# Performance work log

Hardware: AMD Instinct MI355X
Metric: run time of the kernel (lower is better)

Reference implementation:

```python
import jax, jax.numpy as jnp
import numpy as np

N_QUBITS = 4
N_LAYERS = 2
BATCH = 262144


def _apply_ry(psi, theta, wire):
    # psi: (B, 2,2,2,2) real statevector; theta: scalar or (B,)
    c = jnp.reshape(jnp.cos(theta * 0.5), (-1, 1, 1, 1))
    s = jnp.reshape(jnp.sin(theta * 0.5), (-1, 1, 1, 1))
    psi = jnp.moveaxis(psi, wire + 1, 1)
    a, b = psi[:, 0], psi[:, 1]
    psi = jnp.stack([c * a - s * b, s * a + c * b], axis=1)
    return jnp.moveaxis(psi, 1, wire + 1)


def _apply_cnot(psi, ctrl, tgt):
    # flip target amplitude where control bit is 1
    psi = jnp.moveaxis(psi, (ctrl + 1, tgt + 1), (1, 2))
    psi = psi.at[:, 1].set(psi[:, 1, ::-1])
    return jnp.moveaxis(psi, (1, 2), (ctrl + 1, tgt + 1))


def _circuit(encoded, q_params):
    # Batched 4-qubit statevector sim (RY/CNOT are real matrices -> real psi).
    B = encoded.shape[0]
    psi = jnp.zeros((B, 2 ** N_QUBITS), encoded.dtype).at[:, 0].set(1.0)
    psi = psi.reshape((B,) + (2,) * N_QUBITS)  # wire 0 = most significant axis
    for w in range(N_QUBITS):
        psi = _apply_ry(psi, encoded[:, w], w)
    for layer in range(N_LAYERS):
        for i in range(N_QUBITS - 1):
            psi = _apply_cnot(psi, i, i + 1)
        psi = _apply_cnot(psi, N_QUBITS - 1, 0)  # ring closure (n_qubits > 2)
        for i in range(N_QUBITS):
            psi = _apply_ry(psi, q_params[layer * N_QUBITS + i], i)
    p = psi * psi  # probabilities
    zs = []
    for w in range(N_QUBITS):
        pw = jnp.moveaxis(p, w + 1, 1).reshape(B, 2, -1)
        zs.append(pw[:, 0].sum(-1) - pw[:, 1].sum(-1))  # <Z_w>
    return jnp.stack(zs, axis=-1)  # (B, 4)


def setup_inputs() -> dict:
    key = jax.random.key(0)
    ks = jax.random.split(key, 10)
    f32 = jnp.float32
    state = jax.random.normal(ks[0], (BATCH, 64), dtype=f32)
    # state_encoder: Linear(64,32) -> ReLU -> Linear(32,4) -> Tanh
    W1 = jax.random.normal(ks[1], (32, 64), dtype=f32) / np.sqrt(64.0)
    b1 = jnp.zeros((32,), f32)
    W2 = jax.random.normal(ks[2], (N_QUBITS, 32), dtype=f32) / np.sqrt(32.0)
    b2 = jnp.zeros((N_QUBITS,), f32)
    q_params = jax.random.normal(ks[3], (N_LAYERS * N_QUBITS,), dtype=f32) * 0.1
    # q_value_head: Linear(4,32) -> ReLU -> Linear(32,16) -> Tanh
    H1 = jax.random.normal(ks[4], (32, N_QUBITS), dtype=f32) / np.sqrt(float(N_QUBITS))
    c1 = jnp.zeros((32,), f32)
    H2 = jax.random.normal(ks[5], (16, 32), dtype=f32) / np.sqrt(32.0)
    c2 = jnp.zeros((16,), f32)
    return {"state": state, "W1": W1, "b1": b1, "W2": W2, "b2": b2,
            "q_params": q_params, "H1": H1, "c1": c1, "H2": H2, "c2": c2}


def reference(state, W1, b1, W2, b2, q_params, H1, c1, H2, c2):
    B = state.shape[0]
    x = state.reshape(B, -1)
    h = jax.nn.relu(x @ W1.T + b1)
    encoded = jnp.tanh(h @ W2.T + b2)            # (B, 4) rotation angles
    qf = _circuit(encoded, q_params)             # (B, 4) PauliZ expectations
    h2 = jax.nn.relu(qf @ H1.T + c1)
    q_values = jnp.tanh(h2 @ H2.T + c2)          # (B, 16)
    return q_values.reshape(B, 4, 4)
```

## Files before the change

### kernel.cpp

```cpp
#include <hip/hip_runtime.h>
#include <hip/hip_bf16.h>

#define TPB 256
#define BATCH 262144

__device__ __forceinline__ float fast_tanh(float x) {
    float ax = fabsf(x);
    float e  = __expf(-2.0f * ax);
    float t  = (1.0f - e) / (1.0f + e);
    return copysignf(t, x);
}

template <int MASK>
__device__ __forceinline__ void ry_gate(float* psi, float c, float s) {
#pragma unroll
    for (int i = 0; i < 16; i++) {
        if (!(i & MASK)) {
            float a = psi[i], b = psi[i | MASK];
            psi[i]        = c * a - s * b;
            psi[i | MASK] = s * a + c * b;
        }
    }
}

template <int CM, int TM>
__device__ __forceinline__ void cnot_gate(float* psi) {
#pragma unroll
    for (int i = 0; i < 16; i++) {
        if ((i & CM) && !(i & TM)) {
            float t = psi[i];
            psi[i] = psi[i | TM];
            psi[i | TM] = t;
        }
    }
}

__global__ __launch_bounds__(TPB) void qnet_kernel(
    const float* __restrict__ state,
    const float* __restrict__ W1, const float* __restrict__ b1,
    const float* __restrict__ W2, const float* __restrict__ b2,
    const float* __restrict__ qp,
    const float* __restrict__ H1, const float* __restrict__ c1,
    const float* __restrict__ H2, const float* __restrict__ c2,
    float* __restrict__ out)
{
    __shared__ float sW1[2048];
    __shared__ float sb1[32];
    __shared__ float sW2[128];
    __shared__ float sb2[4];
    __shared__ float sH1[128];
    __shared__ float sc1[32];
    __shared__ float sH2[512];
    __shared__ float sc2[16];
    __shared__ float sQc[8], sQs[8];

    const int tid = threadIdx.x;
    for (int i = tid; i < 2048; i += TPB) sW1[i] = W1[i];
    for (int i = tid; i < 512;  i += TPB) sH2[i] = H2[i];
    if (tid < 128) { sW2[tid] = W2[tid]; sH1[tid] = H1[tid]; }
    if (tid < 32)  { sb1[tid] = b1[tid]; sc1[tid] = c1[tid]; }
    if (tid < 16)  { sc2[tid] = c2[tid]; }
    if (tid < 4)   { sb2[tid] = b2[tid]; }
    if (tid < 8) {
        float s, c;
        __sincosf(0.5f * qp[tid], &s, &c);
        sQs[tid] = s; sQc[tid] = c;
    }
    __syncthreads();

    const int bidx = blockIdx.x * TPB + tid;

    float h[32];
#pragma unroll
    for (int j = 0; j < 32; j++) h[j] = sb1[j];

    const float4* x4 = reinterpret_cast<const float4*>(state + (size_t)bidx * 64);

#pragma unroll
    for (int ic = 0; ic < 4; ic++) {
        float4 xr[4];
#pragma unroll
        for (int k = 0; k < 4; k++) xr[k] = x4[ic * 4 + k];

#pragma unroll
        for (int j = 0; j < 32; j++) {
            const float4* w4 = reinterpret_cast<const float4*>(sW1 + j * 64 + ic * 16);
#pragma unroll
            for (int k = 0; k < 4; k++) {
                float4 w = w4[k];
                h[j] = fmaf(xr[k].x, w.x, h[j]);
                h[j] = fmaf(xr[k].y, w.y, h[j]);
                h[j] = fmaf(xr[k].z, w.z, h[j]);
                h[j] = fmaf(xr[k].w, w.w, h[j]);
            }
        }
    }
#pragma unroll
    for (int j = 0; j < 32; j++) h[j] = fmaxf(h[j], 0.0f);

    float e[4];
#pragma unroll
    for (int w = 0; w < 4; w++) {
        float acc = sb2[w];
        const float4* w4 = reinterpret_cast<const float4*>(sW2 + w * 32);
#pragma unroll
        for (int k = 0; k < 8; k++) {
            float4 wv = w4[k];
            acc = fmaf(h[k * 4 + 0], wv.x, acc);
            acc = fmaf(h[k * 4 + 1], wv.y, acc);
            acc = fmaf(h[k * 4 + 2], wv.z, acc);
            acc = fmaf(h[k * 4 + 3], wv.w, acc);
        }
        e[w] = fast_tanh(acc);
    }

    float qf[4];
    {
        float psi[16];
#pragma unroll
        for (int i = 0; i < 16; i++) psi[i] = 0.0f;
        psi[0] = 1.0f;

        float s, c;
        __sincosf(0.5f * e[0], &s, &c); ry_gate<8>(psi, c, s);
        __sincosf(0.5f * e[1], &s, &c); ry_gate<4>(psi, c, s);
        __sincosf(0.5f * e[2], &s, &c); ry_gate<2>(psi, c, s);
        __sincosf(0.5f * e[3], &s, &c); ry_gate<1>(psi, c, s);

#pragma unroll
        for (int layer = 0; layer < 2; layer++) {
            cnot_gate<8, 4>(psi);
            cnot_gate<4, 2>(psi);
            cnot_gate<2, 1>(psi);
            cnot_gate<1, 8>(psi);
            ry_gate<8>(psi, sQc[layer * 4 + 0], sQs[layer * 4 + 0]);
            ry_gate<4>(psi, sQc[layer * 4 + 1], sQs[layer * 4 + 1]);
            ry_gate<2>(psi, sQc[layer * 4 + 2], sQs[layer * 4 + 2]);
            ry_gate<1>(psi, sQc[layer * 4 + 3], sQs[layer * 4 + 3]);
        }

        float p[16];
#pragma unroll
        for (int i = 0; i < 16; i++) p[i] = psi[i] * psi[i];
#pragma unroll
        for (int w = 0; w < 4; w++) {
            const int m = 8 >> w;
            float z = 0.0f;
#pragma unroll
            for (int i = 0; i < 16; i++) z += (i & m) ? -p[i] : p[i];
            qf[w] = z;
        }
    }

    float h2[32];
#pragma unroll
    for (int j = 0; j < 32; j++) {
        const float4 hv = *reinterpret_cast<const float4*>(sH1 + j * 4);
        float a = sc1[j];
        a = fmaf(qf[0], hv.x, a);
        a = fmaf(qf[1], hv.y, a);
        a = fmaf(qf[2], hv.z, a);
        a = fmaf(qf[3], hv.w, a);
        h2[j] = fmaxf(a, 0.0f);
    }

    float qv[16];
#pragma unroll
    for (int o = 0; o < 16; o++) {
        const float4* w4 = reinterpret_cast<const float4*>(sH2 + o * 32);
        float acc = sc2[o];
#pragma unroll
        for (int k = 0; k < 8; k++) {
            float4 wv = w4[k];
            acc = fmaf(h2[k * 4 + 0], wv.x, acc);
            acc = fmaf(h2[k * 4 + 1], wv.y, acc);
            acc = fmaf(h2[k * 4 + 2], wv.z, acc);
            acc = fmaf(h2[k * 4 + 3], wv.w, acc);
        }
        qv[o] = fast_tanh(acc);
    }

    float4* dst = reinterpret_cast<float4*>(out + (size_t)bidx * 16);
#pragma unroll
    for (int k = 0; k < 4; k++) {
        dst[k] = make_float4(qv[k * 4 + 0], qv[k * 4 + 1],
                             qv[k * 4 + 2], qv[k * 4 + 3]);
    }
}

extern "C" void kernel_launch(void* const* d_in, const int* in_sizes, int n_in,
                              void* d_out, int out_size, void* d_ws, size_t ws_size,
                              hipStream_t stream) {
    const float* state = (const float*)d_in[0];
    const float* W1    = (const float*)d_in[1];
    const float* b1    = (const float*)d_in[2];
    const float* W2    = (const float*)d_in[3];
    const float* b2    = (const float*)d_in[4];
    const float* qp    = (const float*)d_in[5];
    const float* H1    = (const float*)d_in[6];
    const float* c1    = (const float*)d_in[7];
    const float* H2    = (const float*)d_in[8];
    const float* c2    = (const float*)d_in[9];
    float* out = (float*)d_out;

    const int blocks = BATCH / TPB;
    qnet_kernel<<<blocks, TPB, 0, stream>>>(state, W1, b1, W2, b2, qp,
                                            H1, c1, H2, c2, out);
}
```

Before: 143.9 us.

## Split each batch row across two threads with shuffle reductions

Each batch row is now handled by a pair of threads. Each thread computes a partial first-layer dot product over half of the 64 inputs and half of the final-layer hidden units, and the partials are combined with xor-1 shuffles. This doubles the thread count and halves per-thread FMA work and register pressure in the linear layers, so more work is available to hide memory latency. In exchange, both threads redundantly compute the second encoder layer and the quantum circuit, and the shuffles add cost. The tanh division is also replaced with a hardware reciprocal.

Result: slower. 156.2 us (+8.6%).

```diff
diff --git a/kernel.cpp b/kernel.cpp
--- a/kernel.cpp
+++ b/kernel.cpp
@@ -7,7 +7,7 @@
 __device__ __forceinline__ float fast_tanh(float x) {
     float ax = fabsf(x);
     float e  = __expf(-2.0f * ax);
-    float t  = (1.0f - e) / (1.0f + e);
+    float t  = (1.0f - e) * __builtin_amdgcn_rcpf(1.0f + e);
     return copysignf(t, x);
 }
 
@@ -68,35 +68,41 @@
     }
     __syncthreads();
 
-    const int bidx = blockIdx.x * TPB + tid;
-
-    float h[32];
-#pragma unroll
-    for (int j = 0; j < 32; j++) h[j] = sb1[j];
-
-    const float4* x4 = reinterpret_cast<const float4*>(state + (size_t)bidx * 64);
-
-#pragma unroll
-    for (int ic = 0; ic < 4; ic++) {
+    const int half = tid & 1;
+    const int row  = blockIdx.x * (TPB / 2) + (tid >> 1);
+
+    const float4* x4 = reinterpret_cast<const float4*>(
+        state + (size_t)row * 64 + half * 32);
+
+    float hp[32];
+#pragma unroll
+    for (int j = 0; j < 32; j++) hp[j] = 0.0f;
+
+#pragma unroll
+    for (int ic = 0; ic < 2; ic++) {
         float4 xr[4];
 #pragma unroll
         for (int k = 0; k < 4; k++) xr[k] = x4[ic * 4 + k];
 
 #pragma unroll
         for (int j = 0; j < 32; j++) {
-            const float4* w4 = reinterpret_cast<const float4*>(sW1 + j * 64 + ic * 16);
+            const float4* w4 = reinterpret_cast<const float4*>(
+                sW1 + j * 64 + half * 32 + ic * 16);
 #pragma unroll
             for (int k = 0; k < 4; k++) {
                 float4 w = w4[k];
-                h[j] = fmaf(xr[k].x, w.x, h[j]);
-                h[j] = fmaf(xr[k].y, w.y, h[j]);
-                h[j] = fmaf(xr[k].z, w.z, h[j]);
-                h[j] = fmaf(xr[k].w, w.w, h[j]);
+                hp[j] = fmaf(xr[k].x, w.x, hp[j]);
+                hp[j] = fmaf(xr[k].y, w.y, hp[j]);
+                hp[j] = fmaf(xr[k].z, w.z, hp[j]);
+                hp[j] = fmaf(xr[k].w, w.w, hp[j]);
             }
         }
     }
-#pragma unroll
-    for (int j = 0; j < 32; j++) h[j] = fmaxf(h[j], 0.0f);
+
+    float h[32];
+#pragma unroll
+    for (int j = 0; j < 32; j++)
+        h[j] = fmaxf(hp[j] + __shfl_xor(hp[j], 1) + sb1[j], 0.0f);
 
     float e[4];
 #pragma unroll
@@ -152,40 +158,48 @@
         }
     }
 
-    float h2[32];
-#pragma unroll
-    for (int j = 0; j < 32; j++) {
+    const int jb = half * 16;
+    float h2[16];
+#pragma unroll
+    for (int jj = 0; jj < 16; jj++) {
+        const int j = jb + jj;
         const float4 hv = *reinterpret_cast<const float4*>(sH1 + j * 4);
         float a = sc1[j];
         a = fmaf(qf[0], hv.x, a);
         a = fmaf(qf[1], hv.y, a);
         a = fmaf(qf[2], hv.z, a);
         a = fmaf(qf[3], hv.w, a);
-        h2[j] = fmaxf(a, 0.0f);
-    }
-
-    float qv[16];
+        h2[jj] = fmaxf(a, 0.0f);
+    }
+
+    float po[16];
 #pragma unroll
     for (int o = 0; o < 16; o++) {
-        const float4* w4 = reinterpret_cast<const float4*>(sH2 + o * 32);
-        float acc = sc2[o];
-#pragma unroll
-        for (int k = 0; k < 8; k++) {
+        const float4* w4 = reinterpret_cast<const float4*>(sH2 + o * 32 + jb);
+        float acc = half ? 0.0f : sc2[o];
+#pragma unroll
+        for (int k = 0; k < 4; k++) {
             float4 wv = w4[k];
             acc = fmaf(h2[k * 4 + 0], wv.x, acc);
             acc = fmaf(h2[k * 4 + 1], wv.y, acc);
             acc = fmaf(h2[k * 4 + 2], wv.z, acc);
             acc = fmaf(h2[k * 4 + 3], wv.w, acc);
         }
-        qv[o] = fast_tanh(acc);
-    }
-
-    float4* dst = reinterpret_cast<float4*>(out + (size_t)bidx * 16);
-#pragma unroll
-    for (int k = 0; k < 4; k++) {
-        dst[k] = make_float4(qv[k * 4 + 0], qv[k * 4 + 1],
-                             qv[k * 4 + 2], qv[k * 4 + 3]);
-    }
+        po[o] = acc;
+    }
+
+    float tot[16];
+#pragma unroll
+    for (int o = 0; o < 16; o++) tot[o] = po[o] + __shfl_xor(po[o], 1);
+
+    const int ob = half * 8;
+    float qv[8];
+#pragma unroll
+    for (int oo = 0; oo < 8; oo++) qv[oo] = fast_tanh(tot[ob + oo]);
+
+    float4* dst = reinterpret_cast<float4*>(out + (size_t)row * 16 + ob);
+    dst[0] = make_float4(qv[0], qv[1], qv[2], qv[3]);
+    dst[1] = make_float4(qv[4], qv[5], qv[6], qv[7]);
 }
 
 extern "C" void kernel_launch(void* const* d_in, const int* in_sizes, int n_in,
@@ -203,7 +217,7 @@
     const float* c2    = (const float*)d_in[9];
     float* out = (float*)d_out;
 
-    const int blocks = BATCH / TPB;
+    const int blocks = BATCH / (TPB / 2);
     qnet_kernel<<<blocks, TPB, 0, stream>>>(state, W1, b1, W2, b2, qp,
                                             H1, c1, H2, c2, out);
 }
```

## Read weights directly via uniform scalar loads instead of staging in LDS

Applied to the files above, without the earlier changes.

Removes the shared-memory staging of all weights and the block barrier. Weights are now read straight from global memory with uniform addresses, which the compiler can turn into scalar (SMEM) loads feeding VALU FMAs as scalar operands, so the per-FMA LDS reads go away. Each thread also loads its whole 64-float input row into registers up front, adds an occupancy hint to launch bounds, and uses a hardware reciprocal in tanh. The risks are scalar-cache pressure from 2K+ weights, higher register use from the 64-element input array, and sincos of the circuit parameters now being recomputed per thread.

After: 138.1 us. 4.0% less time.

```diff
diff --git a/kernel.cpp b/kernel.cpp
--- a/kernel.cpp
+++ b/kernel.cpp
@@ -7,7 +7,7 @@
 __device__ __forceinline__ float fast_tanh(float x) {
     float ax = fabsf(x);
     float e  = __expf(-2.0f * ax);
-    float t  = (1.0f - e) / (1.0f + e);
+    float t  = (1.0f - e) * __builtin_amdgcn_rcpf(1.0f + e);
     return copysignf(t, x);
 }
 
@@ -35,7 +35,7 @@
     }
 }
 
-__global__ __launch_bounds__(TPB) void qnet_kernel(
+__global__ __launch_bounds__(TPB, 4) void qnet_kernel(
     const float* __restrict__ state,
     const float* __restrict__ W1, const float* __restrict__ b1,
     const float* __restrict__ W2, const float* __restrict__ b2,
@@ -44,73 +44,34 @@
     const float* __restrict__ H2, const float* __restrict__ c2,
     float* __restrict__ out)
 {
-    __shared__ float sW1[2048];
-    __shared__ float sb1[32];
-    __shared__ float sW2[128];
-    __shared__ float sb2[4];
-    __shared__ float sH1[128];
-    __shared__ float sc1[32];
-    __shared__ float sH2[512];
-    __shared__ float sc2[16];
-    __shared__ float sQc[8], sQs[8];
+    const int bidx = blockIdx.x * TPB + threadIdx.x;
 
-    const int tid = threadIdx.x;
-    for (int i = tid; i < 2048; i += TPB) sW1[i] = W1[i];
-    for (int i = tid; i < 512;  i += TPB) sH2[i] = H2[i];
-    if (tid < 128) { sW2[tid] = W2[tid]; sH1[tid] = H1[tid]; }
-    if (tid < 32)  { sb1[tid] = b1[tid]; sc1[tid] = c1[tid]; }
-    if (tid < 16)  { sc2[tid] = c2[tid]; }
-    if (tid < 4)   { sb2[tid] = b2[tid]; }
-    if (tid < 8) {
-        float s, c;
-        __sincosf(0.5f * qp[tid], &s, &c);
-        sQs[tid] = s; sQc[tid] = c;
+    const float4* x4 = reinterpret_cast<const float4*>(state + (size_t)bidx * 64);
+    float x[64];
+#pragma unroll
+    for (int k = 0; k < 16; k++) {
+        float4 v = x4[k];
+        x[k * 4 + 0] = v.x; x[k * 4 + 1] = v.y;
+        x[k * 4 + 2] = v.z; x[k * 4 + 3] = v.w;
     }
-    __syncthreads();
-
-    const int bidx = blockIdx.x * TPB + tid;
 
     float h[32];
 #pragma unroll
-    for (int j = 0; j < 32; j++) h[j] = sb1[j];
-
-    const float4* x4 = reinterpret_cast<const float4*>(state + (size_t)bidx * 64);
-
+    for (int j = 0; j < 32; j++) {
+        float acc = b1[j];
 #pragma unroll
-    for (int ic = 0; ic < 4; ic++) {
-        float4 xr[4];
-#pragma unroll
-        for (int k = 0; k < 4; k++) xr[k] = x4[ic * 4 + k];
-
-#pragma unroll
-        for (int j = 0; j < 32; j++) {
-            const float4* w4 = reinterpret_cast<const float4*>(sW1 + j * 64 + ic * 16);
-#pragma unroll
-            for (int k = 0; k < 4; k++) {
-                float4 w = w4[k];
-                h[j] = fmaf(xr[k].x, w.x, h[j]);
-                h[j] = fmaf(xr[k].y, w.y, h[j]);
-                h[j] = fmaf(xr[k].z, w.z, h[j]);
-                h[j] = fmaf(xr[k].w, w.w, h[j]);
-            }
-        }
+        for (int k = 0; k < 64; k++)
+            acc = fmaf(x[k], W1[j * 64 + k], acc);
+        h[j] = fmaxf(acc, 0.0f);
     }
-#pragma unroll
-    for (int j = 0; j < 32; j++) h[j] = fmaxf(h[j], 0.0f);
 
     float e[4];
 #pragma unroll
     for (int w = 0; w < 4; w++) {
-        float acc = sb2[w];
-        const float4* w4 = reinterpret_cast<const float4*>(sW2 + w * 32);
+        float acc = b2[w];
 #pragma unroll
-        for (int k = 0; k < 8; k++) {
-            float4 wv = w4[k];
-            acc = fmaf(h[k * 4 + 0], wv.x, acc);
-            acc = fmaf(h[k * 4 + 1], wv.y, acc);
-            acc = fmaf(h[k * 4 + 2], wv.z, acc);
-            acc = fmaf(h[k * 4 + 3], wv.w, acc);
-        }
+        for (int k = 0; k < 32; k++)
+            acc = fmaf(h[k], W2[w * 32 + k], acc);
         e[w] = fast_tanh(acc);
     }
 
@@ -133,10 +94,15 @@
             cnot_gate<4, 2>(psi);
             cnot_gate<2, 1>(psi);
             cnot_gate<1, 8>(psi);
-            ry_gate<8>(psi, sQc[layer * 4 + 0], sQs[layer * 4 + 0]);
-            ry_gate<4>(psi, sQc[layer * 4 + 1], sQs[layer * 4 + 1]);
-            ry_gate<2>(psi, sQc[layer * 4 + 2], sQs[layer * 4 + 2]);
-            ry_gate<1>(psi, sQc[layer * 4 + 3], sQs[layer * 4 + 3]);
+#pragma unroll
+            for (int i = 0; i < 4; i++) {
+                float s2, c2;
+                __sincosf(0.5f * qp[layer * 4 + i], &s2, &c2);
+                if (i == 0) ry_gate<8>(psi, c2, s2);
+                if (i == 1) ry_gate<4>(psi, c2, s2);
+                if (i == 2) ry_gate<2>(psi, c2, s2);
+                if (i == 3) ry_gate<1>(psi, c2, s2);
+            }
         }
 
         float p[16];
@@ -155,28 +121,21 @@
     float h2[32];
 #pragma unroll
     for (int j = 0; j < 32; j++) {
-        const float4 hv = *reinterpret_cast<const float4*>(sH1 + j * 4);
-        float a = sc1[j];
-        a = fmaf(qf[0], hv.x, a);
-        a = fmaf(qf[1], hv.y, a);
-        a = fmaf(qf[2], hv.z, a);
-        a = fmaf(qf[3], hv.w, a);
+        float a = c1[j];
+        a = fmaf(qf[0], H1[j * 4 + 0], a);
+        a = fmaf(qf[1], H1[j * 4 + 1], a);
+        a = fmaf(qf[2], H1[j * 4 + 2], a);
+        a = fmaf(qf[3], H1[j * 4 + 3], a);
         h2[j] = fmaxf(a, 0.0f);
     }
 
     float qv[16];
 #pragma unroll
     for (int o = 0; o < 16; o++) {
-        const float4* w4 = reinterpret_cast<const float4*>(sH2 + o * 32);
-        float acc = sc2[o];
+        float acc = c2[o];
 #pragma unroll
-        for (int k = 0; k < 8; k++) {
-            float4 wv = w4[k];
-            acc = fmaf(h2[k * 4 + 0], wv.x, acc);
-            acc = fmaf(h2[k * 4 + 1], wv.y, acc);
-            acc = fmaf(h2[k * 4 + 2], wv.z, acc);
-            acc = fmaf(h2[k * 4 + 3], wv.w, acc);
-        }
+        for (int k = 0; k < 32; k++)
+            acc = fmaf(h2[k], H2[o * 32 + k], acc);
         qv[o] = fast_tanh(acc);
     }
 
```
